# Performance work log

Measured on AMD Instinct MI355X. Metric: run time of the kernel, lower is better.

The kernel has to match this reference:

```python
import jax, jax.numpy as jnp
import numpy as np

DEP_NUM, HEAD_NUM, BSZ, DIM, REL = 96, 96, 16, 512, 128


def setup_inputs() -> dict:
    key = jax.random.key(0)
    k1, k2, k3, k4 = jax.random.split(key, 4)
    outs = jax.random.normal(k1, (DEP_NUM, BSZ, DIM), dtype=jnp.float32)
    graph_state = jax.random.normal(k2, (HEAD_NUM, BSZ, DIM), dtype=jnp.float32)
    # nn.init.normal_(std=0.02) for both weights, zero biases
    Wt = 0.02 * jax.random.normal(k3, (DIM, 2 * DIM), dtype=jnp.float32)
    bt = jnp.zeros((DIM,), dtype=jnp.float32)
    Wp = 0.02 * jax.random.normal(k4, (REL, DIM), dtype=jnp.float32)
    bp = jnp.zeros((REL,), dtype=jnp.float32)
    return {"outs": outs, "graph_state": graph_state, "Wt": Wt, "bt": bt, "Wp": Wp, "bp": bp}


def reference(outs, graph_state, Wt, bt, Wp, bp):
    # outs: [dep, b, D], graph_state: [head, b, D]
    # Linear(cat(dep, head)) == dep @ Wt[:, :D].T + head @ Wt[:, D:].T + bt
    D = outs.shape[-1]
    dep_proj = jnp.einsum('dbi,ei->dbe', outs, Wt[:, :D])           # [dep, b, D]
    head_proj = jnp.einsum('hbi,ei->hbe', graph_state, Wt[:, D:])   # [head, b, D]
    # broadcast-sum to pairwise: [dep, b, head, D]
    h = jax.nn.relu(dep_proj[:, :, None, :] + jnp.swapaxes(head_proj, 0, 1)[None] + bt)
    # dropout: identity in eval mode
    scores = jnp.einsum('dbhe,re->dbhr', h, Wp) + bp                # [dep, b, head, REL]
    nil = jnp.zeros(scores.shape[:-1] + (1,), dtype=scores.dtype)
    scores = jnp.concatenate([nil, scores], axis=-1)                # [dep, b, head, REL+1]
    return jax.nn.log_softmax(scores, axis=-1)
```

## Files before the change

### kernel.cpp

```cpp
#include <hip/hip_runtime.h>
#include <math.h>

#define DEP   96
#define HEADS 96
#define BSZ   16
#define DIM   512
#define REL   128
#define RELP  129

typedef __attribute__((ext_vector_type(8))) _Float16  half8;
typedef __attribute__((ext_vector_type(2))) __fp16    fp16x2;
typedef __attribute__((ext_vector_type(4))) float     floatx4;

__device__ __forceinline__ unsigned short f2h(float x) {
    union { _Float16 h; unsigned short u; } c;
    c.h = (_Float16)x;
    return c.u;
}
__device__ __forceinline__ unsigned pk_f2h(float a, float b) {
    union { fp16x2 h; unsigned u; } c;
    c.h = __builtin_amdgcn_cvt_pkrtz(a, b);
    return c.u;
}
__device__ __forceinline__ unsigned pk_add_h2(unsigned a, unsigned b) {
    unsigned r; asm("v_pk_add_f16 %0, %1, %2" : "=v"(r) : "v"(a), "v"(b)); return r;
}
__device__ __forceinline__ unsigned pk_max_h2(unsigned a, unsigned b) {
    unsigned r; asm("v_pk_max_f16 %0, %1, %2" : "=v"(r) : "v"(a), "v"(b)); return r;
}

#define PSS 72

__global__ __launch_bounds__(256) void proj_kernel(
    const float* __restrict__ outs, const float* __restrict__ graph,
    const float* __restrict__ Wt, const float* __restrict__ bt,
    const float* __restrict__ Wp,
    float* __restrict__ P1, unsigned short* __restrict__ P2H,
    unsigned short* __restrict__ WpH)
{
    {
        const int fb = (blockIdx.z * gridDim.y + blockIdx.y) * gridDim.x + blockIdx.x;
        if (fb < 32) {
            const int c = fb * 256 + (int)threadIdx.x;
            float4 a = *(const float4*)(Wp + (size_t)c * 8);
            float4 b = *(const float4*)(Wp + (size_t)c * 8 + 4);
            uint4 o;
            o.x = pk_f2h(a.x, a.y); o.y = pk_f2h(a.z, a.w);
            o.z = pk_f2h(b.x, b.y); o.w = pk_f2h(b.z, b.w);
            *(uint4*)(WpH + (size_t)c * 8) = o;
        }
    }

    const int z = blockIdx.z;
    const float* A = z ? graph : outs;
    const int off  = z ? DIM : 0;
    const int row0 = blockIdx.y * 32;
    const int col0 = blockIdx.x * 64;

    __shared__ __align__(16) unsigned short As[32 * PSS];
    __shared__ __align__(16) unsigned short Ws[64 * PSS];

    const int tid  = threadIdx.x;
    const int lane = tid & 63;
    const int wv   = tid >> 6;
    const int ln15 = lane & 15;
    const int quad = lane >> 4;
    const int mh   = wv & 1;
    const int nh   = wv >> 1;

    floatx4 acc[2];
    acc[0] = (floatx4){0.f,0.f,0.f,0.f};
    acc[1] = (floatx4){0.f,0.f,0.f,0.f};

    for (int kt = 0; kt < DIM; kt += 64) {
        {
            const int r  = tid >> 3;
            const int e8 = (tid & 7) * 8;
            const float* p = A + (size_t)(row0 + r) * DIM + kt + e8;
            float4 va = *(const float4*)p;
            float4 vb = *(const float4*)(p + 4);
            uint4 o;
            o.x = pk_f2h(va.x, va.y); o.y = pk_f2h(va.z, va.w);
            o.z = pk_f2h(vb.x, vb.y); o.w = pk_f2h(vb.z, vb.w);
            *(uint4*)&As[r * PSS + e8] = o;
        }
        #pragma unroll
        for (int q = 0; q < 2; ++q) {
            const int slot = q*256 + tid;
            const int r  = slot >> 3;
            const int e8 = (slot & 7) * 8;
            const float* p = Wt + (size_t)(col0 + r) * (2*DIM) + off + kt + e8;
            float4 va = *(const float4*)p;
            float4 vb = *(const float4*)(p + 4);
            uint4 o;
            o.x = pk_f2h(va.x, va.y); o.y = pk_f2h(va.z, va.w);
            o.z = pk_f2h(vb.x, vb.y); o.w = pk_f2h(vb.z, vb.w);
            *(uint4*)&Ws[r * PSS + e8] = o;
        }
        __syncthreads();
        #pragma unroll
        for (int ks = 0; ks < 64; ks += 32) {
            half8 af = *(const half8*)&As[(mh*16 + ln15) * PSS + ks + quad*8];
            #pragma unroll
            for (int nt = 0; nt < 2; ++nt) {
                half8 bf8 = *(const half8*)&Ws[(nh*32 + nt*16 + ln15) * PSS + ks + quad*8];
                acc[nt] = __builtin_amdgcn_mfma_f32_16x16x32_f16(af, bf8, acc[nt], 0, 0, 0);
            }
        }
        __syncthreads();
    }

    #pragma unroll
    for (int nt = 0; nt < 2; ++nt) {
        #pragma unroll
        for (int reg = 0; reg < 4; ++reg) {
            const int m = row0 + mh*16 + quad*4 + reg;
            const int n = col0 + nh*32 + nt*16 + ln15;
            float v = acc[nt][reg];
            if (!z) P1[(size_t)m * DIM + n] = v + bt[n];
            else    P2H[(size_t)m * DIM + n] = f2h(v);
        }
    }
}

#define HSS 72
#define WSS 72

__global__ __launch_bounds__(256, 4) void fused_kernel(
    const float* __restrict__ P1, const unsigned short* __restrict__ P2H,
    const unsigned short* __restrict__ WpH, const float* __restrict__ bp,
    float* __restrict__ out)
{
    const int db = blockIdx.x;
    const int b  = db & 15;

    __shared__ __align__(16) char arena[96*HSS*2 + 128*WSS*2];
    unsigned short* hs = (unsigned short*)arena;
    unsigned short* ws = (unsigned short*)(arena + 96*HSS*2);
    float* outb = (float*)arena;

    __shared__ __align__(16) unsigned short drowH[DIM];
    __shared__ float pmx[96][2];
    __shared__ float pl [96][2];
    __shared__ float lseS[96];

    const int tid  = threadIdx.x;
    const int lane = tid & 63;
    const int wv   = tid >> 6;
    const int ln15 = lane & 15;
    const int quad = lane >> 4;
    const int mh   = wv & 1;
    const int nh   = wv >> 1;

    {
        float2 v = *(const float2*)(P1 + (size_t)db * DIM + tid*2);
        *(unsigned*)&drowH[tid*2] = pk_f2h(v.x, v.y);
    }
    __syncthreads();

    floatx4 acc[3][4];
    #pragma unroll
    for (int i = 0; i < 3; ++i)
        #pragma unroll
        for (int j = 0; j < 4; ++j) acc[i][j] = (floatx4){0.f,0.f,0.f,0.f};

    for (int kt = 0; kt < DIM; kt += 64) {
        #pragma unroll
        for (int q = 0; q < 3; ++q) {
            const int slot = q*256 + tid;
            const int h  = slot >> 3;
            const int e8 = (slot & 7) * 8;
            uint4 pv = *(const uint4*)(P2H + ((size_t)h * BSZ + b) * DIM + kt + e8);
            uint4 dv = *(const uint4*)&drowH[kt + e8];
            uint4 o;
            o.x = pk_max_h2(pk_add_h2(pv.x, dv.x), 0u);
            o.y = pk_max_h2(pk_add_h2(pv.y, dv.y), 0u);
            o.z = pk_max_h2(pk_add_h2(pv.z, dv.z), 0u);
            o.w = pk_max_h2(pk_add_h2(pv.w, dv.w), 0u);
            *(uint4*)&hs[h * HSS + e8] = o;
        }
        #pragma unroll
        for (int q = 0; q < 4; ++q) {
            const int slot = q*256 + tid;
            const int r = slot >> 3;
            const int g = (slot & 7) * 8;
            *(uint4*)&ws[r * WSS + g] =
                *(const uint4*)(WpH + (size_t)r * DIM + kt + g);
        }
        __syncthreads();

        #pragma unroll
        for (int ks = 0; ks < 64; ks += 32) {
            half8 af[3], bf[4];
            #pragma unroll
            for (int mt = 0; mt < 3; ++mt)
                af[mt] = *(const half8*)&hs[(mh*48 + mt*16 + ln15) * HSS + ks + quad*8];
            #pragma unroll
            for (int nt = 0; nt < 4; ++nt)
                bf[nt] = *(const half8*)&ws[(nh*64 + nt*16 + ln15) * WSS + ks + quad*8];
            #pragma unroll
            for (int nt = 0; nt < 4; ++nt)
                #pragma unroll
                for (int mt = 0; mt < 3; ++mt)
                    acc[mt][nt] = __builtin_amdgcn_mfma_f32_16x16x32_f16(
                        af[mt], bf[nt], acc[mt][nt], 0, 0, 0);
        }
        __syncthreads();
    }

    float bpv[4];
    #pragma unroll
    for (int nt = 0; nt < 4; ++nt) bpv[nt] = bp[nh*64 + nt*16 + ln15];

    #pragma unroll
    for (int mt = 0; mt < 3; ++mt) {
        #pragma unroll
        for (int reg = 0; reg < 4; ++reg) {
            const int m = mh*48 + mt*16 + quad*4 + reg;
            float s[4];
            #pragma unroll
            for (int nt = 0; nt < 4; ++nt) s[nt] = acc[mt][nt][reg] + bpv[nt];
            float mx = fmaxf(fmaxf(s[0], s[1]), fmaxf(s[2], s[3]));
            #pragma unroll
            for (int msk = 1; msk < 16; msk <<= 1) mx = fmaxf(mx, __shfl_xor(mx, msk));
            float l = 0.f;
            #pragma unroll
            for (int nt = 0; nt < 4; ++nt) l += __expf(s[nt] - mx);
            #pragma unroll
            for (int msk = 1; msk < 16; msk <<= 1) l += __shfl_xor(l, msk);
            if (ln15 == 0) { pmx[m][nh] = mx; pl[m][nh] = l; }
        }
    }
    __syncthreads();

    if (tid < 96) {
        const float mx0 = pmx[tid][0], mx1 = pmx[tid][1];
        const float MX = fmaxf(fmaxf(mx0, mx1), 0.f);
        const float L  = pl[tid][0] * __expf(mx0 - MX) + pl[tid][1] * __expf(mx1 - MX)
                       + __expf(-MX);
        lseS[tid] = MX + __logf(L);
    }
    __syncthreads();

    #pragma unroll
    for (int g = 0; g < 2; ++g) {
        if (mh == g) {
            #pragma unroll
            for (int mt = 0; mt < 3; ++mt) {
                #pragma unroll
                for (int reg = 0; reg < 4; ++reg) {
                    const int lrow = mt*16 + quad*4 + reg;
                    const float lse = lseS[g*48 + lrow];
                    #pragma unroll
                    for (int nt = 0; nt < 4; ++nt)
                        outb[lrow*RELP + 1 + nh*64 + nt*16 + ln15] =
                            acc[mt][nt][reg] + bpv[nt] - lse;
                    if (nh == 0 && ln15 == 0) outb[lrow*RELP] = -lse;
                }
            }
        }
        __syncthreads();
        float4* gout = (float4*)(out + (size_t)db * (HEADS*RELP) + g * (48*RELP));
        const float4* lsrc = (const float4*)outb;
        for (int j = tid; j < 1548; j += 256)
            gout[j] = lsrc[j];
        __syncthreads();
    }
}

extern "C" void kernel_launch(void* const* d_in, const int* in_sizes, int n_in,
                              void* d_out, int out_size, void* d_ws, size_t ws_size,
                              hipStream_t stream) {
    const float* outs  = (const float*)d_in[0];
    const float* graph = (const float*)d_in[1];
    const float* Wt    = (const float*)d_in[2];
    const float* bt    = (const float*)d_in[3];
    const float* Wp    = (const float*)d_in[4];
    const float* bp    = (const float*)d_in[5];
    float* out = (float*)d_out;

    float* P1           = (float*)d_ws;
    unsigned short* P2H = (unsigned short*)(P1 + 786432);
    unsigned short* WpH = P2H + 786432;

    proj_kernel<<<dim3(DIM/64, (DEP*BSZ)/32, 2), 256, 0, stream>>>(
        outs, graph, Wt, bt, Wp, P1, P2H, WpH);
    fused_kernel<<<DEP*BSZ, 256, 0, stream>>>(P1, P2H, WpH, bp, out);
}
```

Measured before the change: 141.7 us.

## Pre-swizzle Wp into MFMA fragment order and load B fragments directly from global

```diff
diff --git a/kernel.cpp b/kernel.cpp
--- a/kernel.cpp
+++ b/kernel.cpp
@@ -36,18 +36,24 @@
     const float* __restrict__ Wt, const float* __restrict__ bt,
     const float* __restrict__ Wp,
     float* __restrict__ P1, unsigned short* __restrict__ P2H,
-    unsigned short* __restrict__ WpH)
+    unsigned short* __restrict__ WpF)
 {
     {
         const int fb = (blockIdx.z * gridDim.y + blockIdx.y) * gridDim.x + blockIdx.x;
         if (fb < 32) {
-            const int c = fb * 256 + (int)threadIdx.x;
-            float4 a = *(const float4*)(Wp + (size_t)c * 8);
-            float4 b = *(const float4*)(Wp + (size_t)c * 8 + 4);
+            const int c    = fb * 256 + (int)threadIdx.x;
+            const int ln   = c & 63;
+            const int nq   = (c >> 6) & 7;
+            const int kk   = c >> 9;
+            const int row  = (nq >> 2) * 64 + (nq & 3) * 16 + (ln & 15);
+            const int col  = kk * 32 + ((ln >> 4) & 3) * 8;
+            const float* src = Wp + (size_t)row * DIM + col;
+            float4 a = *(const float4*)src;
+            float4 b = *(const float4*)(src + 4);
             uint4 o;
             o.x = pk_f2h(a.x, a.y); o.y = pk_f2h(a.z, a.w);
             o.z = pk_f2h(b.x, b.y); o.w = pk_f2h(b.z, b.w);
-            *(uint4*)(WpH + (size_t)c * 8) = o;
+            *(uint4*)(WpF + (size_t)c * 8) = o;
         }
     }
 
@@ -124,21 +130,16 @@
 }
 
 #define HSS 72
-#define WSS 72
 
 __global__ __launch_bounds__(256, 4) void fused_kernel(
     const float* __restrict__ P1, const unsigned short* __restrict__ P2H,
-    const unsigned short* __restrict__ WpH, const float* __restrict__ bp,
+    const unsigned short* __restrict__ WpF, const float* __restrict__ bp,
     float* __restrict__ out)
 {
     const int db = blockIdx.x;
     const int b  = db & 15;
 
-    __shared__ __align__(16) char arena[96*HSS*2 + 128*WSS*2];
-    unsigned short* hs = (unsigned short*)arena;
-    unsigned short* ws = (unsigned short*)(arena + 96*HSS*2);
-    float* outb = (float*)arena;
-
+    __shared__ __align__(16) unsigned short hs[96 * HSS];
     __shared__ __align__(16) unsigned short drowH[DIM];
     __shared__ float pmx[96][2];
     __shared__ float pl [96][2];
@@ -151,6 +152,7 @@
     const int quad = lane >> 4;
     const int mh   = wv & 1;
     const int nh   = wv >> 1;
+    const int e8   = (tid & 7) * 8;
 
     {
         float2 v = *(const float2*)(P1 + (size_t)db * DIM + tid*2);
@@ -164,14 +166,22 @@
         #pragma unroll
         for (int j = 0; j < 4; ++j) acc[i][j] = (floatx4){0.f,0.f,0.f,0.f};
 
-    for (int kt = 0; kt < DIM; kt += 64) {
+    for (int kti = 0; kti < 8; ++kti) {
+        const int kt = kti * 64;
+
+        half8 bf[2][4];
+        #pragma unroll
+        for (int ks = 0; ks < 2; ++ks)
+            #pragma unroll
+            for (int nt = 0; nt < 4; ++nt)
+                bf[ks][nt] = *(const half8*)(WpF +
+                    (size_t)((((kti*2 + ks)*8 + nh*4 + nt)*64 + lane)) * 8);
+
+        uint4 dv = *(const uint4*)&drowH[kt + e8];
         #pragma unroll
         for (int q = 0; q < 3; ++q) {
-            const int slot = q*256 + tid;
-            const int h  = slot >> 3;
-            const int e8 = (slot & 7) * 8;
+            const int h = (q*256 + tid) >> 3;
             uint4 pv = *(const uint4*)(P2H + ((size_t)h * BSZ + b) * DIM + kt + e8);
-            uint4 dv = *(const uint4*)&drowH[kt + e8];
             uint4 o;
             o.x = pk_max_h2(pk_add_h2(pv.x, dv.x), 0u);
             o.y = pk_max_h2(pk_add_h2(pv.y, dv.y), 0u);
@@ -179,31 +189,20 @@
             o.w = pk_max_h2(pk_add_h2(pv.w, dv.w), 0u);
             *(uint4*)&hs[h * HSS + e8] = o;
         }
-        #pragma unroll
-        for (int q = 0; q < 4; ++q) {
-            const int slot = q*256 + tid;
-            const int r = slot >> 3;
-            const int g = (slot & 7) * 8;
-            *(uint4*)&ws[r * WSS + g] =
-                *(const uint4*)(WpH + (size_t)r * DIM + kt + g);
-        }
-        __syncthreads();
-
-        #pragma unroll
-        for (int ks = 0; ks < 64; ks += 32) {
-            half8 af[3], bf[4];
+        __syncthreads();
+
+        #pragma unroll
+        for (int ks = 0; ks < 2; ++ks) {
+            half8 af[3];
             #pragma unroll
             for (int mt = 0; mt < 3; ++mt)
-                af[mt] = *(const half8*)&hs[(mh*48 + mt*16 + ln15) * HSS + ks + quad*8];
-            #pragma unroll
-            for (int nt = 0; nt < 4; ++nt)
-                bf[nt] = *(const half8*)&ws[(nh*64 + nt*16 + ln15) * WSS + ks + quad*8];
+                af[mt] = *(const half8*)&hs[(mh*48 + mt*16 + ln15) * HSS + ks*32 + quad*8];
             #pragma unroll
             for (int nt = 0; nt < 4; ++nt)
                 #pragma unroll
                 for (int mt = 0; mt < 3; ++mt)
                     acc[mt][nt] = __builtin_amdgcn_mfma_f32_16x16x32_f16(
-                        af[mt], bf[nt], acc[mt][nt], 0, 0, 0);
+                        af[mt], bf[ks][nt], acc[mt][nt], 0, 0, 0);
         }
         __syncthreads();
     }
@@ -243,28 +242,17 @@
     __syncthreads();
 
     #pragma unroll
-    for (int g = 0; g < 2; ++g) {
-        if (mh == g) {
-            #pragma unroll
-            for (int mt = 0; mt < 3; ++mt) {
-                #pragma unroll
-                for (int reg = 0; reg < 4; ++reg) {
-                    const int lrow = mt*16 + quad*4 + reg;
-                    const float lse = lseS[g*48 + lrow];
-                    #pragma unroll
-                    for (int nt = 0; nt < 4; ++nt)
-                        outb[lrow*RELP + 1 + nh*64 + nt*16 + ln15] =
-                            acc[mt][nt][reg] + bpv[nt] - lse;
-                    if (nh == 0 && ln15 == 0) outb[lrow*RELP] = -lse;
-                }
-            }
-        }
-        __syncthreads();
-        float4* gout = (float4*)(out + (size_t)db * (HEADS*RELP) + g * (48*RELP));
-        const float4* lsrc = (const float4*)outb;
-        for (int j = tid; j < 1548; j += 256)
-            gout[j] = lsrc[j];
-        __syncthreads();
+    for (int mt = 0; mt < 3; ++mt) {
+        #pragma unroll
+        for (int reg = 0; reg < 4; ++reg) {
+            const int m = mh*48 + mt*16 + quad*4 + reg;
+            const float lse = lseS[m];
+            const size_t base = ((size_t)db * HEADS + m) * RELP;
+            #pragma unroll
+            for (int nt = 0; nt < 4; ++nt)
+                out[base + 1 + nh*64 + nt*16 + ln15] = acc[mt][nt][reg] + bpv[nt] - lse;
+            if (nh == 0 && ln15 == 0) out[base] = -lse;
+        }
     }
 }
 
@@ -281,9 +269,9 @@
 
     float* P1           = (float*)d_ws;
     unsigned short* P2H = (unsigned short*)(P1 + 786432);
-    unsigned short* WpH = P2H + 786432;
+    unsigned short* WpF = P2H + 786432;
 
     proj_kernel<<<dim3(DIM/64, (DEP*BSZ)/32, 2), 256, 0, stream>>>(
-        outs, graph, Wt, bt, Wp, P1, P2H, WpH);
-    fused_kernel<<<DEP*BSZ, 256, 0, stream>>>(P1, P2H, WpH, bp, out);
-}
+        outs, graph, Wt, bt, Wp, P1, P2H, WpF);
+    fused_kernel<<<DEP*BSZ, 256, 0, stream>>>(P1, P2H, WpF, bp, out);
+}
```

After: 147.0 us. +3.8%, slower.
